# Optimization experiments

Hardware: AMD Instinct MI355X
Metric: run time of the kernel (lower is better)

The kernel has to match this reference:

```python
import jax, jax.numpy as jnp
import numpy as np

# ---------------- Chu-Liu-Edmonds MST decode (faithful numpy port) ----------------

def _find_cycle(parents, length, current_nodes):
    added = [False] * length
    added[0] = True
    cycle = set()
    has_cycle = False
    for i in range(1, length):
        if has_cycle:
            break
        if added[i] or not current_nodes[i]:
            continue
        this_cycle = {i}
        added[i] = True
        has_cycle = True
        next_node = i
        while parents[next_node] not in this_cycle:
            next_node = parents[next_node]
            if added[next_node]:
                has_cycle = False
                break
            added[next_node] = True
            this_cycle.add(next_node)
        if has_cycle:
            original = next_node
            cycle.add(original)
            next_node = parents[original]
            while next_node != original:
                cycle.add(next_node)
                next_node = parents[next_node]
            break
    return has_cycle, list(cycle)


def chu_liu_edmonds(length, score_matrix, current_nodes, final_edges, old_input, old_output, representatives):
    parents = [-1]
    for node1 in range(1, length):
        parents.append(0)
        if current_nodes[node1]:
            max_score = score_matrix[0, node1]
            for node2 in range(1, length):
                if node2 == node1 or not current_nodes[node2]:
                    continue
                new_score = score_matrix[node2, node1]
                if new_score > max_score:
                    max_score = new_score
                    parents[node1] = node2
    has_cycle, cycle = _find_cycle(parents, length, current_nodes)
    if not has_cycle:
        final_edges[0] = -1
        for node in range(1, length):
            if not current_nodes[node]:
                continue
            parent = old_input[parents[node], node]
            child = old_output[parents[node], node]
            final_edges[child] = parent
        return
    cycle_weight = 0.0
    for node in cycle:
        cycle_weight += score_matrix[parents[node], node]
    cycle_representative = cycle[0]
    for node in range(length):
        if not current_nodes[node] or node in cycle:
            continue
        in_edge_weight = float('-inf')
        in_edge = -1
        out_edge_weight = float('-inf')
        out_edge = -1
        for node_in_cycle in cycle:
            if score_matrix[node_in_cycle, node] > in_edge_weight:
                in_edge_weight = score_matrix[node_in_cycle, node]
                in_edge = node_in_cycle
            score = cycle_weight + score_matrix[node, node_in_cycle] - score_matrix[parents[node_in_cycle], node_in_cycle]
            if score > out_edge_weight:
                out_edge_weight = score
                out_edge = node_in_cycle
        score_matrix[cycle_representative, node] = in_edge_weight
        old_input[cycle_representative, node] = old_input[in_edge, node]
        old_output[cycle_representative, node] = old_output[in_edge, node]
        score_matrix[node, cycle_representative] = out_edge_weight
        old_output[node, cycle_representative] = old_output[node, out_edge]
        old_input[node, cycle_representative] = old_input[node, out_edge]
    considered = []
    for i, node_in_cycle in enumerate(cycle):
        considered.append(set())
        if i > 0:
            current_nodes[node_in_cycle] = False
        for node in representatives[node_in_cycle]:
            considered[i].add(node)
            if i > 0:
                representatives[cycle_representative].add(node)
    chu_liu_edmonds(length, score_matrix, current_nodes, final_edges, old_input, old_output, representatives)
    found = False
    key_node = -1
    for i, node in enumerate(cycle):
        for cycle_rep in considered[i]:
            if cycle_rep in final_edges:
                key_node = node
                found = True
                break
        if found:
            break
    previous = parents[key_node]
    while previous != key_node:
        child = old_output[parents[previous], previous]
        parent = old_input[parents[previous], previous]
        final_edges[child] = parent
        previous = parents[previous]


def decode_mst(energy, length):
    # energy: numpy [num_labels, T, T]
    max_length = energy.shape[-1]
    energy = energy[:, :length, :length]
    label_id_matrix = energy.argmax(axis=0)
    score_matrix = np.array(energy.max(axis=0), copy=True)
    old_input = np.zeros([length, length], dtype=np.int32)
    old_output = np.zeros([length, length], dtype=np.int32)
    current_nodes = [True] * length
    representatives = []
    for node1 in range(length):
        score_matrix[node1, node1] = 0.0
        representatives.append({node1})
        for node2 in range(node1 + 1, length):
            old_input[node1, node2] = node1
            old_output[node1, node2] = node2
            old_input[node2, node1] = node2
            old_output[node2, node1] = node1
    final_edges = {}
    chu_liu_edmonds(length, score_matrix, current_nodes, final_edges, old_input, old_output, representatives)
    heads = np.zeros([max_length], np.int32)
    head_type = np.ones([max_length], np.int32)
    for child, parent in final_edges.items():
        heads[child] = parent
        head_type[child] = label_id_matrix[parent, child]
    return heads, head_type


# ---------------- biaffine scoring (jax) ----------------

@jax.jit
def _energy(encoded_text, W_head_arc, b_head_arc, W_dep_arc, b_dep_arc, U_arc,
            W_head_lab, b_head_lab, W_dep_lab, b_dep_lab, U_lab):
    h_arc = jax.nn.elu(encoded_text @ W_head_arc + b_head_arc)   # [B,T,A]
    d_arc = jax.nn.elu(encoded_text @ W_dep_arc + b_dep_arc)     # [B,T,A]
    arc_scores = jnp.einsum('bia,ac,bjc->bij', h_arc, U_arc, d_arc)  # head i -> dep j
    h_lab = jax.nn.elu(encoded_text @ W_head_lab + b_head_lab)   # [B,T,R]
    d_lab = jax.nn.elu(encoded_text @ W_dep_lab + b_dep_lab)     # [B,T,R]
    lab_scores = jnp.einsum('bir,lrs,bjs->blij', h_lab, U_lab, d_lab)  # [B,L,T,T]
    norm_arc = jax.nn.log_softmax(arc_scores, axis=1)   # normalize over heads
    norm_lab = jax.nn.log_softmax(lab_scores, axis=1)   # normalize over labels
    return jnp.exp(norm_arc[:, None, :, :] + norm_lab)  # [B,L,T,T] edge energies


def setup_inputs() -> dict:
    key = jax.random.key(0)
    ks = jax.random.split(key, 8)
    B, T, D, A, R, L = 32, 128, 768, 512, 128, 50
    s = 0.02
    return {
        'encoded_text': jax.random.normal(ks[0], (B, T, D), jnp.float32),
        'W_head_arc': jax.random.normal(ks[1], (D, A), jnp.float32) * s,
        'b_head_arc': jnp.zeros((A,), jnp.float32),
        'W_dep_arc': jax.random.normal(ks[2], (D, A), jnp.float32) * s,
        'b_dep_arc': jnp.zeros((A,), jnp.float32),
        'U_arc': jax.random.normal(ks[3], (A, A), jnp.float32) * s,
        'W_head_lab': jax.random.normal(ks[4], (D, R), jnp.float32) * s,
        'b_head_lab': jnp.zeros((R,), jnp.float32),
        'W_dep_lab': jax.random.normal(ks[5], (D, R), jnp.float32) * s,
        'b_dep_lab': jnp.zeros((R,), jnp.float32),
        'U_lab': jax.random.normal(ks[6], (L, R, R), jnp.float32) * s,
        'mask': jnp.ones((B, T), jnp.bool_),
    }


def reference(encoded_text, W_head_arc, b_head_arc, W_dep_arc, b_dep_arc, U_arc,
              W_head_lab, b_head_lab, W_dep_lab, b_dep_lab, U_lab, mask):
    energy = _energy(encoded_text, W_head_arc, b_head_arc, W_dep_arc, b_dep_arc, U_arc,
                     W_head_lab, b_head_lab, W_dep_lab, b_dep_lab, U_lab)
    lengths = np.asarray(mask.sum(-1))
    energy_np = np.asarray(energy)
    heads, tags = [], []
    # per-example Chu-Liu-Edmonds decode (inherently sequential, as in the original)
    for i in range(energy_np.shape[0]):
        h, t = decode_mst(energy_np[i], int(lengths[i]))
        heads.append(h)
        tags.append(t)
    return energy, jnp.asarray(np.stack(heads)), jnp.asarray(np.stack(tags))
```

## Files before the change

### kernel.cpp

```cpp
#include <hip/hip_runtime.h>
#include <math.h>

#define B_ 32
#define T_ 128
#define D_ 768
#define A_ 512
#define R_ 128
#define L_ 50

__global__ __launch_bounds__(256)
void proj_gemm_k(const float* __restrict__ X,
                 const float* __restrict__ Wha, const float* __restrict__ bha,
                 const float* __restrict__ Wda, const float* __restrict__ bda,
                 const float* __restrict__ Whl, const float* __restrict__ bhl,
                 const float* __restrict__ Wdl, const float* __restrict__ bdl,
                 float* __restrict__ HA, float* __restrict__ DA,
                 float* __restrict__ HL, float* __restrict__ DL)
{
    __shared__ float As[16][68];
    __shared__ float Bs[16][132];
    const int bx = blockIdx.x;
    const float *W, *bias; float* C; int ld, ncol;
    if (bx < 4)      { W = Wha; bias = bha; C = HA; ld = 512; ncol = bx * 128; }
    else if (bx < 8) { W = Wda; bias = bda; C = DA; ld = 512; ncol = (bx - 4) * 128; }
    else if (bx == 8){ W = Whl; bias = bhl; C = HL; ld = 128; ncol = 0; }
    else             { W = Wdl; bias = bdl; C = DL; ld = 128; ncol = 0; }
    const int m0 = blockIdx.y * 64;
    const int tid = threadIdx.x;
    const int tx = tid & 15, ry = tid >> 4;
    float acc[4][8] = {};
    for (int k0 = 0; k0 < 768; k0 += 16) {
        {
            int row = tid >> 2, kb = (tid & 3) * 4;
            float4 a = *(const float4*)&X[(size_t)(m0 + row) * 768 + k0 + kb];
            As[kb + 0][row] = a.x; As[kb + 1][row] = a.y;
            As[kb + 2][row] = a.z; As[kb + 3][row] = a.w;
        }
        {
            int kk = tid >> 4, c0 = (tid & 15) * 4;
            const float* Bp = &W[(size_t)(k0 + kk) * ld + ncol + c0];
            *(float4*)&Bs[kk][c0] = *(const float4*)&Bp[0];
            *(float4*)&Bs[kk][c0 + 64] = *(const float4*)&Bp[64];
        }
        __syncthreads();
#pragma unroll
        for (int kk = 0; kk < 16; ++kk) {
            float4 a4 = *(const float4*)&As[kk][ry * 4];
            float4 b0 = *(const float4*)&Bs[kk][tx * 4];
            float4 b1 = *(const float4*)&Bs[kk][tx * 4 + 64];
            float av[4] = { a4.x, a4.y, a4.z, a4.w };
            float bv[8] = { b0.x, b0.y, b0.z, b0.w, b1.x, b1.y, b1.z, b1.w };
#pragma unroll
            for (int i = 0; i < 4; ++i)
#pragma unroll
                for (int j = 0; j < 8; ++j)
                    acc[i][j] += av[i] * bv[j];
        }
        __syncthreads();
    }
    float bv0[8];
    {
        float4 q0 = *(const float4*)&bias[ncol + tx * 4];
        float4 q1 = *(const float4*)&bias[ncol + tx * 4 + 64];
        bv0[0] = q0.x; bv0[1] = q0.y; bv0[2] = q0.z; bv0[3] = q0.w;
        bv0[4] = q1.x; bv0[5] = q1.y; bv0[6] = q1.z; bv0[7] = q1.w;
    }
#pragma unroll
    for (int i = 0; i < 4; ++i) {
        int m = m0 + ry * 4 + i;
        size_t base = (size_t)m * ld + ncol;
        float o[8];
#pragma unroll
        for (int j = 0; j < 8; ++j) {
            float v = acc[i][j] + bv0[j];
            o[j] = v > 0.0f ? v : expm1f(v);
        }
        float4 s0 = { o[0], o[1], o[2], o[3] };
        float4 s1 = { o[4], o[5], o[6], o[7] };
        *(float4*)&C[base + tx * 4] = s0;
        *(float4*)&C[base + tx * 4 + 64] = s1;
    }
}

__global__ __launch_bounds__(256)
void gemm_k(const float* __restrict__ A, const float* __restrict__ B,
            const float* __restrict__ bias, float* __restrict__ C,
            int K, int lda, int ldb, int ldc,
            long long sA, long long sB, long long sC, long long c_outer, int flags)
{
    __shared__ float As[16][68];
    __shared__ float Bs[16][132];
    A += (size_t)blockIdx.z * sA;
    B += (size_t)blockIdx.z * sB;
    C += (size_t)blockIdx.z * sC;
    const int m0 = blockIdx.y * 64, n0 = blockIdx.x * 128;
    const int tid = threadIdx.x;
    const int tx = tid & 15, ry = tid >> 4;
    float acc[4][8] = {};
    for (int k0 = 0; k0 < K; k0 += 16) {
        {
            int row = tid >> 2, kb = (tid & 3) * 4;
            float4 a = *(const float4*)&A[(size_t)(m0 + row) * lda + k0 + kb];
            As[kb + 0][row] = a.x; As[kb + 1][row] = a.y;
            As[kb + 2][row] = a.z; As[kb + 3][row] = a.w;
        }
        if (!(flags & 4)) {
            int kk = tid >> 4, c0 = (tid & 15) * 4;
            const float* Bp = &B[(size_t)(k0 + kk) * ldb + n0 + c0];
            *(float4*)&Bs[kk][c0] = *(const float4*)&Bp[0];
            *(float4*)&Bs[kk][c0 + 64] = *(const float4*)&Bp[64];
        } else {
            int col = tid >> 1, kb = (tid & 1) * 8;
            const float* Bp = &B[(size_t)(n0 + col) * ldb + k0 + kb];
            float4 b0 = *(const float4*)&Bp[0];
            float4 b1 = *(const float4*)&Bp[4];
            Bs[kb + 0][col] = b0.x; Bs[kb + 1][col] = b0.y;
            Bs[kb + 2][col] = b0.z; Bs[kb + 3][col] = b0.w;
            Bs[kb + 4][col] = b1.x; Bs[kb + 5][col] = b1.y;
            Bs[kb + 6][col] = b1.z; Bs[kb + 7][col] = b1.w;
        }
        __syncthreads();
#pragma unroll
        for (int kk = 0; kk < 16; ++kk) {
            float4 a4 = *(const float4*)&As[kk][ry * 4];
            float4 b0 = *(const float4*)&Bs[kk][tx * 4];
            float4 b1 = *(const float4*)&Bs[kk][tx * 4 + 64];
            float av[4] = { a4.x, a4.y, a4.z, a4.w };
            float bv[8] = { b0.x, b0.y, b0.z, b0.w, b1.x, b1.y, b1.z, b1.w };
#pragma unroll
            for (int i = 0; i < 4; ++i)
#pragma unroll
                for (int j = 0; j < 8; ++j)
                    acc[i][j] += av[i] * bv[j];
        }
        __syncthreads();
    }
    float bv0[8] = {};
    if (flags & 1) {
        float4 q0 = *(const float4*)&bias[n0 + tx * 4];
        float4 q1 = *(const float4*)&bias[n0 + tx * 4 + 64];
        bv0[0] = q0.x; bv0[1] = q0.y; bv0[2] = q0.z; bv0[3] = q0.w;
        bv0[4] = q1.x; bv0[5] = q1.y; bv0[6] = q1.z; bv0[7] = q1.w;
    }
#pragma unroll
    for (int i = 0; i < 4; ++i) {
        int m = m0 + ry * 4 + i;
        size_t base = (size_t)(m >> 7) * c_outer + (size_t)(m & 127) * ldc + n0;
        float o[8];
#pragma unroll
        for (int j = 0; j < 8; ++j) {
            float v = acc[i][j] + bv0[j];
            if (flags & 2) v = v > 0.0f ? v : expm1f(v);
            o[j] = v;
        }
        float4 s0 = { o[0], o[1], o[2], o[3] };
        float4 s1 = { o[4], o[5], o[6], o[7] };
        *(float4*)&C[base + tx * 4] = s0;
        *(float4*)&C[base + tx * 4 + 64] = s1;
    }
}

__global__ __launch_bounds__(256)
void transpose_k(const float* __restrict__ in, float* __restrict__ out)
{
    __shared__ float tile[32][33];
    int b = blockIdx.z;
    int bx = blockIdx.x, by = blockIdx.y;
    int tx = threadIdx.x, ty = threadIdx.y;
    const float* src = in + (size_t)b * T_ * R_;
    float* dst = out + (size_t)b * T_ * R_;
#pragma unroll
    for (int r = 0; r < 4; ++r)
        tile[ty + 8 * r][tx] = src[(size_t)(by * 32 + ty + 8 * r) * 128 + bx * 32 + tx];
    __syncthreads();
#pragma unroll
    for (int r = 0; r < 4; ++r)
        dst[(size_t)(bx * 32 + ty + 8 * r) * 128 + by * 32 + tx] = tile[tx][ty + 8 * r];
}

__global__ __launch_bounds__(128)
void arc_logsoftmax_k(float* __restrict__ arc)
{
    int b = blockIdx.x, j = threadIdx.x;
    float* base = arc + (size_t)b * T_ * T_ + j;
    float m = -INFINITY;
    for (int i = 0; i < T_; ++i) m = fmaxf(m, base[(size_t)i * T_]);
    float s = 0.0f;
    for (int i = 0; i < T_; ++i) s += expf(base[(size_t)i * T_] - m);
    float ls = m + logf(s);
    for (int i = 0; i < T_; ++i) base[(size_t)i * T_] -= ls;
}

__global__ __launch_bounds__(256)
void tl_lab_k(const float* __restrict__ HL, const float* __restrict__ Ul,
              const float* __restrict__ dlt, float* __restrict__ E)
{
    __shared__ float Ts[128 * 68];
    __shared__ float As[16][68];
    __shared__ float Bs[16][132];
    const int l = blockIdx.x, b = blockIdx.y;
    const int m0 = blockIdx.z * 64;
    const int tid = threadIdx.x;
    const int tx = tid & 15, ry = tid >> 4;
    const float* Apan = HL + (size_t)b * 16384 + (size_t)m0 * 128;
    const float* Bpan = Ul + (size_t)l * 16384;
    const float* Dpan = dlt + (size_t)b * 16384;
    float acc[4][8] = {};
    for (int k0 = 0; k0 < 128; k0 += 16) {
        {
            int row = tid >> 2, kb = (tid & 3) * 4;
            float4 a = *(const float4*)&Apan[(size_t)row * 128 + k0 + kb];
            As[kb + 0][row] = a.x; As[kb + 1][row] = a.y;
            As[kb + 2][row] = a.z; As[kb + 3][row] = a.w;
        }
        {
            int kk = tid >> 4, c0 = (tid & 15) * 4;
            const float* Bp = &Bpan[(size_t)(k0 + kk) * 128 + c0];
            *(float4*)&Bs[kk][c0] = *(const float4*)&Bp[0];
            *(float4*)&Bs[kk][c0 + 64] = *(const float4*)&Bp[64];
        }
        __syncthreads();
#pragma unroll
        for (int kk = 0; kk < 16; ++kk) {
            float4 a4 = *(const float4*)&As[kk][ry * 4];
            float4 b0 = *(const float4*)&Bs[kk][tx * 4];
            float4 b1 = *(const float4*)&Bs[kk][tx * 4 + 64];
            float av[4] = { a4.x, a4.y, a4.z, a4.w };
            float bv[8] = { b0.x, b0.y, b0.z, b0.w, b1.x, b1.y, b1.z, b1.w };
#pragma unroll
            for (int i = 0; i < 4; ++i)
#pragma unroll
                for (int j = 0; j < 8; ++j)
                    acc[i][j] += av[i] * bv[j];
        }
        __syncthreads();
    }
#pragma unroll
    for (int j = 0; j < 8; ++j) {
        int col = (j < 4) ? (tx * 4 + j) : (64 + tx * 4 + j - 4);
        float4 w = { acc[0][j], acc[1][j], acc[2][j], acc[3][j] };
        *(float4*)&Ts[col * 68 + ry * 4] = w;
#pragma unroll
        for (int i = 0; i < 4; ++i) acc[i][j] = 0.0f;
    }
    __syncthreads();
    for (int k0 = 0; k0 < 128; k0 += 16) {
        {
            int kk = tid >> 4, c0 = (tid & 15) * 4;
            const float* Bp = &Dpan[(size_t)(k0 + kk) * 128 + c0];
            *(float4*)&Bs[kk][c0] = *(const float4*)&Bp[0];
            *(float4*)&Bs[kk][c0 + 64] = *(const float4*)&Bp[64];
        }
        __syncthreads();
#pragma unroll
        for (int kk = 0; kk < 16; ++kk) {
            float4 a4 = *(const float4*)&Ts[(k0 + kk) * 68 + ry * 4];
            float4 b0 = *(const float4*)&Bs[kk][tx * 4];
            float4 b1 = *(const float4*)&Bs[kk][tx * 4 + 64];
            float av[4] = { a4.x, a4.y, a4.z, a4.w };
            float bv[8] = { b0.x, b0.y, b0.z, b0.w, b1.x, b1.y, b1.z, b1.w };
#pragma unroll
            for (int i = 0; i < 4; ++i)
#pragma unroll
                for (int j = 0; j < 8; ++j)
                    acc[i][j] += av[i] * bv[j];
        }
        __syncthreads();
    }
    float* base = E + ((size_t)b * L_ + l) * 16384 + (size_t)m0 * 128;
#pragma unroll
    for (int i = 0; i < 4; ++i) {
        float4 s0 = { acc[i][0], acc[i][1], acc[i][2], acc[i][3] };
        float4 s1 = { acc[i][4], acc[i][5], acc[i][6], acc[i][7] };
        *(float4*)&base[(size_t)(ry * 4 + i) * 128 + tx * 4] = s0;
        *(float4*)&base[(size_t)(ry * 4 + i) * 128 + tx * 4 + 64] = s1;
    }
}

__global__ __launch_bounds__(256)
void energy_combine_k(float* __restrict__ E, const float* __restrict__ narc,
                      float* __restrict__ score_g, unsigned char* __restrict__ labmax_g)
{
    int g = blockIdx.x * 256 + threadIdx.x;
    int b = g >> 14;
    int ij = g & 16383;
    float* base = E + (size_t)b * L_ * T_ * T_ + ij;
    float v[L_];
    float m = -INFINITY;
    int am = 0;
#pragma unroll
    for (int l = 0; l < L_; ++l) {
        v[l] = base[(size_t)l * T_ * T_];
        if (v[l] > m) { m = v[l]; am = l; }
    }
    float s = 0.0f;
#pragma unroll
    for (int l = 0; l < L_; ++l) s += expf(v[l] - m);
    float ls = m + logf(s);
    float na = narc[(size_t)b * T_ * T_ + ij];
#pragma unroll
    for (int l = 0; l < L_; ++l) base[(size_t)l * T_ * T_] = expf(na + v[l] - ls);
    int i = ij >> 7, j = ij & 127;
    score_g[(size_t)b * 16384 + ij] = (i == j) ? 0.0f : expf(na + m - ls);
    labmax_g[(size_t)b * 16384 + ij] = (unsigned char)am;
}

__global__ __launch_bounds__(256)
void mst_k(const float* __restrict__ score_g, const unsigned char* __restrict__ labmax_g,
           float* __restrict__ heads, float* __restrict__ tags)
{
    const int b = blockIdx.x, t = threadIdx.x;
    __shared__ float score[128 * 129];
    __shared__ unsigned short oio[128 * 129];
    __shared__ unsigned char pstL[96 * 128];
    __shared__ unsigned char kynL[96 * 128];
    __shared__ int parents[128];
    __shared__ int fe[128];
    __shared__ float pmx[128];
    __shared__ int pp[128];
    __shared__ float cwacc[128];
    __shared__ int cnt[128];
    __shared__ int offarr[128];
    __shared__ float Lsub[128];
    __shared__ unsigned char Lnode[128], Lcid[128];
    __shared__ unsigned char cidarr[128], oncyc[128];

    {
        const float4* src = (const float4*)(score_g + (size_t)b * 16384);
        for (int i = t; i < 4096; i += 256) {
            float4 v = src[i];
            int r = i >> 5, c = (i & 31) * 4;
            float* d = &score[r * 129 + c];
            d[0] = v.x; d[1] = v.y; d[2] = v.z; d[3] = v.w;
        }
    }
    for (int i = t; i < 16384; i += 256) {
        int r = i >> 7, c = i & 127;
        oio[r * 129 + c] = (unsigned short)(r | (c << 8));
    }
    if (t < 128) { fe[t] = -2; oncyc[t] = 0; }
    __syncthreads();
    if (t < 128) score[t * 129 + t] = -INFINITY;
    __syncthreads();
    float mxl = 0.0f; int pl = 0;
    if (t >= 128) {
        int col = t - 128;
        float mx = -INFINITY; int pu = 64;
        if (col != 0) {
            mx = score[64 * 129 + col];
#pragma unroll 16
            for (int n2 = 65; n2 < 128; ++n2) {
                float sc = score[n2 * 129 + col];
                if (sc > mx) { mx = sc; pu = n2; }
            }
        }
        pmx[col] = mx; pp[col] = pu;
    } else if (t != 0) {
        mxl = score[t]; pl = 0;
#pragma unroll 16
        for (int n2 = 1; n2 < 64; ++n2) {
            float sc = score[n2 * 129 + t];
            if (sc > mxl) { mxl = sc; pl = n2; }
        }
    }
    __syncthreads();
    if (t == 0) parents[0] = -1;
    else if (t < 128) parents[t] = (pmx[t] > mxl) ? pp[t] : pl;
    __syncthreads();

    if (t < 64) {
        const int n0 = t, n1 = t + 64;
        int p0 = parents[n0], p1 = parents[n1];
        int c0 = 1, c1 = 1;
        int r0 = n0, r1 = n1;
        int lev = 0, nact = 128, pass = 0;
        for (;;) {
            int rounds = 32 - __clz(nact - 1);
            int a0 = (n0 == 0 || !c0) ? 0 : p0;
            int a1 = (!c1) ? 0 : p1;
            int m0 = n0, m1 = n1;
            for (int s = 0; s < rounds; ++s) {
                int pk0 = (a0 << 7) | m0;
                int pk1 = (a1 << 7) | m1;
                int q00 = __shfl(pk0, a0 & 63, 64);
                int q01 = __shfl(pk1, a0 & 63, 64);
                int q10 = __shfl(pk0, a1 & 63, 64);
                int q11 = __shfl(pk1, a1 & 63, 64);
                int g0 = (a0 & 64) ? q01 : q00;
                int g1 = (a1 & 64) ? q11 : q10;
                a0 = g0 >> 7; int gm0 = g0 & 127; m0 = gm0 < m0 ? gm0 : m0;
                a1 = g1 >> 7; int gm1 = g1 & 127; m1 = gm1 < m1 ? gm1 : m1;
            }
            int pred0 = (n0 >= 1) && c0 && (a0 != 0);
            int pred1 = c1 && (a1 != 0);
            unsigned long long bal0 = __ballot(pred0);
            unsigned long long bal1 = __ballot(pred1);
            if (bal0 == 0ull && bal1 == 0ull) {
                if (n0 == 0) fe[0] = -1;
                else if (c0) { int w = oio[p0 * 129 + n0]; fe[w >> 8] = w & 255; }
                if (c1) { int w = oio[p1 * 129 + n1]; fe[w >> 8] = w & 255; }
                __threadfence_block();
                break;
            }
            unsigned char ep = (unsigned char)(++pass);
            if (pred0) oncyc[a0] = ep;
            if (pred1) oncyc[a1] = ep;
            cnt[n0] = 0; cnt[n1] = 0;
            cwacc[n0] = 0.0f; cwacc[n1] = 0.0f;
            __threadfence_block();
            int onc0 = c0 && (oncyc[n0] == ep);
            int onc1 = c1 && (oncyc[n1] == ep);
            const int cid0 = m0, cid1 = m1;
            cidarr[n0] = onc0 ? (unsigned char)cid0 : 0xFF;
            cidarr[n1] = onc1 ? (unsigned char)cid1 : 0xFF;
            float sub0 = 0.0f, sub1 = 0.0f;
            int rk0 = 0, rk1 = 0;
            if (onc0) { sub0 = score[p0 * 129 + n0]; rk0 = atomicAdd(&cnt[cid0], 1); atomicAdd(&cwacc[cid0], sub0); }
            if (onc1) { sub1 = score[p1 * 129 + n1]; rk1 = atomicAdd(&cnt[cid1], 1); atomicAdd(&cwacc[cid1], sub1); }
            __threadfence_block();
            int x0 = cnt[n0], x1 = cnt[n1];
            int v = (x0 & 0xFFFF) | (x1 << 16);
            for (int off = 1; off < 64; off <<= 1) {
                int u = __shfl(v, t >= off ? t - off : 0, 64);
                v += (t >= off) ? u : 0;
            }
            int tot = __shfl(v, 63, 64);
            int Mtot = (tot & 0xFFFF) + (tot >> 16);
            offarr[n0] = (v & 0xFFFF) - x0;
            offarr[n1] = (tot & 0xFFFF) + ((v >> 16) & 0xFFFF) - x1;
            __threadfence_block();
            if (onc0) { int sl = offarr[cid0] + rk0; Lnode[sl] = (unsigned char)n0; Lcid[sl] = (unsigned char)cid0; Lsub[sl] = sub0; }
            if (onc1) { int sl = offarr[cid1] + rk1; Lnode[sl] = (unsigned char)n1; Lcid[sl] = (unsigned char)cid1; Lsub[sl] = sub1; }
            int rc0 = cidarr[r0], rc1 = cidarr[r1];
            if (lev < 96) {
                pstL[lev * 128 + n0] = (unsigned char)p0;
                pstL[lev * 128 + n1] = (unsigned char)p1;
                kynL[lev * 128 + n0] = (rc0 != 0xFF) ? (unsigned char)r0 : 0xFF;
                kynL[lev * 128 + n1] = (rc1 != 0xFF) ? (unsigned char)r1 : 0xFF;
            }
            if (rc0 != 0xFF) r0 = rc0;
            if (rc1 != 0xFF) r1 = rc1;
            __threadfence_block();
            {
                int lim0 = c0 ? (onc0 ? cid0 : 256) : -1;
                int lim1 = c1 ? (onc1 ? cid1 : 256) : -1;
                float inw0 = -INFINITY, outw0 = -INFINITY;
                float inw1 = -INFINITY, outw1 = -INFINITY;
                int qi0 = 0, qo0 = 0, qi1 = 0, qo1 = 0;
                int cidC = Lcid[0], mC = Lnode[0];
                float sbC = Lsub[0];
                for (int i = 0; i < Mtot; ++i) {
                    int cidN = 0, mN = 0; float sbN = 0.0f;
                    if (i + 1 < Mtot) { cidN = Lcid[i + 1]; mN = Lnode[i + 1]; sbN = Lsub[i + 1]; }
                    if (cidC < lim0) {
                        float si = score[mC * 129 + n0];
                        float so = score[n0 * 129 + mC] - sbC;
                        int wi = oio[mC * 129 + n0];
                        int wo = oio[n0 * 129 + mC];
                        if (si > inw0) { inw0 = si; qi0 = wi; }
                        if (so > outw0) { outw0 = so; qo0 = wo; }
                    }
                    if (cidC < lim1) {
                        float si = score[mC * 129 + n1];
                        float so = score[n1 * 129 + mC] - sbC;
                        int wi = oio[mC * 129 + n1];
                        int wo = oio[n1 * 129 + mC];
                        if (si > inw1) { inw1 = si; qi1 = wi; }
                        if (so > outw1) { outw1 = so; qo1 = wo; }
                    }
                    int segend = (i + 1 == Mtot) || (cidN != cidC);
                    if (segend) {
                        if (cidC < lim0) {
                            float cwc = cwacc[cidC];
                            score[cidC * 129 + n0] = inw0; oio[cidC * 129 + n0] = (unsigned short)qi0;
                            score[n0 * 129 + cidC] = cwc + outw0; oio[n0 * 129 + cidC] = (unsigned short)qo0;
                        }
                        if (cidC < lim1) {
                            float cwc = cwacc[cidC];
                            score[cidC * 129 + n1] = inw1; oio[cidC * 129 + n1] = (unsigned short)qi1;
                            score[n1 * 129 + cidC] = cwc + outw1; oio[n1 * 129 + cidC] = (unsigned short)qo1;
                        }
                        inw0 = -INFINITY; outw0 = -INFINITY;
                        inw1 = -INFINITY; outw1 = -INFINITY;
                    }
                    cidC = cidN; mC = mN; sbC = sbN;
                }
            }
            __threadfence_block();
            int rp0 = onc0 && (n0 == cid0);
            int rp1 = onc1 && (n1 == cid1);
            unsigned long long q0 = __ballot(rp0);
            unsigned long long q1 = __ballot(rp1);
            int ncyc = (int)__popcll(q0) + (int)__popcll(q1);
            if (ncyc >= 2) {
                float inw0 = -INFINITY, outw0 = -INFINITY;
                float inw1 = -INFINITY, outw1 = -INFINITY;
                int qi0 = 0, qo0 = 0, qi1 = 0, qo1 = 0;
                int cidC = Lcid[0], mC = Lnode[0];
                float sbC = Lsub[0];
                for (int i = 0; i < Mtot; ++i) {
                    int cidN = 0, mN = 0; float sbN = 0.0f;
                    if (i + 1 < Mtot) { cidN = Lcid[i + 1]; mN = Lnode[i + 1]; sbN = Lsub[i + 1]; }
                    int e0 = rp0 && (cidC > cid0);
                    int e1 = rp1 && (cidC > cid1);
                    if (e0) {
                        float si = score[mC * 129 + n0];
                        float so = score[n0 * 129 + mC] - sbC;
                        int wi = oio[mC * 129 + n0];
                        int wo = oio[n0 * 129 + mC];
                        if (si > inw0) { inw0 = si; qi0 = wi; }
                        if (so > outw0) { outw0 = so; qo0 = wo; }
                    }
                    if (e1) {
                        float si = score[mC * 129 + n1];
                        float so = score[n1 * 129 + mC] - sbC;
                        int wi = oio[mC * 129 + n1];
                        int wo = oio[n1 * 129 + mC];
                        if (si > inw1) { inw1 = si; qi1 = wi; }
                        if (so > outw1) { outw1 = so; qo1 = wo; }
                    }
                    int segend = (i + 1 == Mtot) || (cidN != cidC);
                    if (segend) {
                        if (e0) {
                            float cwc = cwacc[cidC];
                            score[cidC * 129 + n0] = inw0; oio[cidC * 129 + n0] = (unsigned short)qi0;
                            score[n0 * 129 + cidC] = cwc + outw0; oio[n0 * 129 + cidC] = (unsigned short)qo0;
                        }
                        if (e1) {
                            float cwc = cwacc[cidC];
                            score[cidC * 129 + n1] = inw1; oio[cidC * 129 + n1] = (unsigned short)qi1;
                            score[n1 * 129 + cidC] = cwc + outw1; oio[n1 * 129 + cidC] = (unsigned short)qo1;
                        }
                        inw0 = -INFINITY; outw0 = -INFINITY;
                        inw1 = -INFINITY; outw1 = -INFINITY;
                    }
                    cidC = cidN; mC = mN; sbC = sbN;
                }
                __threadfence_block();
            }
            if (onc0 && n0 != cid0) c0 = 0;
            if (onc1 && n1 != cid1) c1 = 0;
            if (c0 && n0 != 0) { int cp = cidarr[p0]; if (cp != 0xFF) p0 = cp; }
            if (c1)            { int cp = cidarr[p1]; if (cp != 0xFF) p1 = cp; }
            {
                unsigned long long w0 = q0, w1 = q1;
                while (w0 | w1) {
                    int repA, repB = -1;
                    if (w0) { repA = (int)__ffsll((long long)w0) - 1; w0 &= w0 - 1; }
                    else    { repA = 64 + (int)__ffsll((long long)w1) - 1; w1 &= w1 - 1; }
                    if (w0) { repB = (int)__ffsll((long long)w0) - 1; w0 &= w0 - 1; }
                    else if (w1) { repB = 64 + (int)__ffsll((long long)w1) - 1; w1 &= w1 - 1; }
                    float aA = c0 ? score[n0 * 129 + repA] : -INFINITY;
                    float bA = c1 ? score[n1 * 129 + repA] : -INFINITY;
                    float aB = -INFINITY, bB = -INFINITY;
                    if (repB >= 0) {
                        aB = c0 ? score[n0 * 129 + repB] : -INFINITY;
                        bB = c1 ? score[n1 * 129 + repB] : -INFINITY;
                    }
                    float vA; int iA;
                    if (bA > aA) { vA = bA; iA = n1; } else { vA = aA; iA = n0; }
                    float vB; int iB;
                    if (bB > aB) { vB = bB; iB = n1; } else { vB = aB; iB = n0; }
#pragma unroll
                    for (int off = 32; off >= 1; off >>= 1) {
                        float oA = __shfl_xor(vA, off, 64);
                        int jA = __shfl_xor(iA, off, 64);
                        float oB = __shfl_xor(vB, off, 64);
                        int jB = __shfl_xor(iB, off, 64);
                        if (oA > vA || (oA == vA && jA < iA)) { vA = oA; iA = jA; }
                        if (oB > vB || (oB == vB && jB < iB)) { vB = oB; iB = jB; }
                    }
                    if (n0 == repA) p0 = iA;
                    if (n1 == repA) p1 = iA;
                    if (repB >= 0) {
                        if (n0 == repB) p0 = iB;
                        if (n1 == repB) p1 = iB;
                    }
                }
            }
            nact -= (Mtot - ncyc);
            ++lev;
        }
        int ltop = lev < 96 ? lev : 96;
        for (int l2 = ltop - 1; l2 >= 0; --l2) {
            int ky0 = kynL[l2 * 128 + n0], ky1 = kynL[l2 * 128 + n1];
            int cand0 = (ky0 != 0xFF) && (fe[n0] != -2);
            int cand1 = (ky1 != 0xFF) && (fe[n1] != -2);
            if (cand0) {
                int key = ky0;
                int prev = pstL[l2 * 128 + key];
                int guard = 0;
                while (prev != key && guard++ < 130) {
                    int pp2 = pstL[l2 * 128 + prev];
                    int w = oio[pp2 * 129 + prev];
                    fe[w >> 8] = w & 255;
                    prev = pp2;
                }
            }
            if (cand1) {
                int key = ky1;
                int prev = pstL[l2 * 128 + key];
                int guard = 0;
                while (prev != key && guard++ < 130) {
                    int pp2 = pstL[l2 * 128 + prev];
                    int w = oio[pp2 * 129 + prev];
                    fe[w >> 8] = w & 255;
                    prev = pp2;
                }
            }
            __threadfence_block();
        }
    }
    __syncthreads();

    if (t < 128) {
        int f = fe[t];
        float h, ht;
        if (f != -2) {
            h = (float)f;
            int prow = (f < 0) ? 127 : f;
            ht = (float)(int)labmax_g[(size_t)b * 16384 + prow * 128 + t];
        } else { h = 0.0f; ht = 1.0f; }
        heads[b * 128 + t] = h;
        tags[b * 128 + t] = ht;
    }
}

extern "C" void kernel_launch(void* const* d_in, const int* in_sizes, int n_in,
                              void* d_out, int out_size, void* d_ws, size_t ws_size,
                              hipStream_t stream)
{
    const float* X   = (const float*)d_in[0];
    const float* Wha = (const float*)d_in[1];
    const float* bha = (const float*)d_in[2];
    const float* Wda = (const float*)d_in[3];
    const float* bda = (const float*)d_in[4];
    const float* Ua  = (const float*)d_in[5];
    const float* Whl = (const float*)d_in[6];
    const float* bhl = (const float*)d_in[7];
    const float* Wdl = (const float*)d_in[8];
    const float* bdl = (const float*)d_in[9];
    const float* Ul  = (const float*)d_in[10];

    char* ws = (char*)d_ws;
    float* HA    = (float*)(ws + (size_t)0);
    float* DA    = (float*)(ws + ((size_t)8 << 20));
    float* TA    = (float*)(ws + ((size_t)16 << 20));
    float* HL    = (float*)(ws + ((size_t)24 << 20));
    float* DL    = (float*)(ws + ((size_t)26 << 20));
    float* DLt   = (float*)(ws + ((size_t)28 << 20));
    float* ARC   = (float*)(ws + ((size_t)30 << 20));
    float* SCORE = (float*)(ws + ((size_t)32 << 20));
    unsigned char* LABMAX = (unsigned char*)(ws + ((size_t)34 << 20));

    float* E     = (float*)d_out;
    float* heads = E + (size_t)B_ * L_ * T_ * T_;
    float* tags  = heads + (size_t)B_ * T_;

    dim3 thr(256);
    proj_gemm_k<<<dim3(10, 64), thr, 0, stream>>>(X, Wha, bha, Wda, bda, Whl, bhl, Wdl, bdl,
                                                  HA, DA, HL, DL);
    gemm_k<<<dim3(4, 64, 1), thr, 0, stream>>>(HA, Ua, nullptr, TA, 512, 512, 512, 512, 0, 0, 0, (long long)128 * 512, 0);
    transpose_k<<<dim3(4, 4, 32), dim3(32, 8), 0, stream>>>(DL, DLt);
    gemm_k<<<dim3(1, 2, 32), thr, 0, stream>>>(TA, DA, nullptr, ARC, 512, 512, 512, 128, 65536, 65536, 16384, 0, 4);
    arc_logsoftmax_k<<<32, 128, 0, stream>>>(ARC);
    tl_lab_k<<<dim3(50, 32, 2), thr, 0, stream>>>(HL, Ul, DLt, E);
    energy_combine_k<<<2048, 256, 0, stream>>>(E, ARC, SCORE, LABMAX);
    mst_k<<<32, 256, 0, stream>>>(SCORE, LABMAX, heads, tags);
}
```

Measured before the change: 882.6 us.

## Unroll contraction scan by four and compute new cycle-rep parents per lane

Packs the per-member node and cycle-id lists into one 16-bit array padded with sentinel entries. The contraction scans are unrolled by four with all shared-memory loads issued up front, to expose memory-level parallelism. Parent selection for new cycle representatives changes from a wave-wide shuffle reduction per pair of reps to one lane per representative doing a serial 128-entry column scan. A compacted representative list is built with ballots. This trades shuffle reductions for per-lane serial loops and adds register pressure and redundant loads past segment ends.

After: 1.242 ms. 1.41x slower.

```diff
diff --git a/kernel.cpp b/kernel.cpp
--- a/kernel.cpp
+++ b/kernel.cpp
@@ -321,9 +321,9 @@
     __shared__ float cwacc[128];
     __shared__ int cnt[128];
     __shared__ int offarr[128];
-    __shared__ float Lsub[128];
-    __shared__ unsigned char Lnode[128], Lcid[128];
-    __shared__ unsigned char cidarr[128], oncyc[128];
+    __shared__ float Lsub[136];
+    __shared__ unsigned short Lpk[136];
+    __shared__ unsigned char cidarr[128], oncyc[128], replist[72];
 
     {
         const float4* src = (const float4*)(score_g + (size_t)b * 16384);
@@ -374,6 +374,7 @@
         int c0 = 1, c1 = 1;
         int r0 = n0, r1 = n1;
         int lev = 0, nact = 128, pass = 0;
+        const unsigned long long lmask = (1ull << t) - 1ull;
         for (;;) {
             int rounds = 32 - __clz(nact - 1);
             int a0 = (n0 == 0 || !c0) ? 0 : p0;
@@ -413,6 +414,13 @@
             const int cid0 = m0, cid1 = m1;
             cidarr[n0] = onc0 ? (unsigned char)cid0 : 0xFF;
             cidarr[n1] = onc1 ? (unsigned char)cid1 : 0xFF;
+            int rp0 = onc0 && (n0 == cid0);
+            int rp1 = onc1 && (n1 == cid1);
+            unsigned long long q0 = __ballot(rp0);
+            unsigned long long q1 = __ballot(rp1);
+            int ncyc = (int)__popcll(q0) + (int)__popcll(q1);
+            if (rp0) replist[(int)__popcll(q0 & lmask)] = (unsigned char)n0;
+            if (rp1) replist[(int)__popcll(q0) + (int)__popcll(q1 & lmask)] = (unsigned char)n1;
             float sub0 = 0.0f, sub1 = 0.0f;
             int rk0 = 0, rk1 = 0;
             if (onc0) { sub0 = score[p0 * 129 + n0]; rk0 = atomicAdd(&cnt[cid0], 1); atomicAdd(&cwacc[cid0], sub0); }
@@ -429,8 +437,9 @@
             offarr[n0] = (v & 0xFFFF) - x0;
             offarr[n1] = (tot & 0xFFFF) + ((v >> 16) & 0xFFFF) - x1;
             __threadfence_block();
-            if (onc0) { int sl = offarr[cid0] + rk0; Lnode[sl] = (unsigned char)n0; Lcid[sl] = (unsigned char)cid0; Lsub[sl] = sub0; }
-            if (onc1) { int sl = offarr[cid1] + rk1; Lnode[sl] = (unsigned char)n1; Lcid[sl] = (unsigned char)cid1; Lsub[sl] = sub1; }
+            if (onc0) { int sl = offarr[cid0] + rk0; Lpk[sl] = (unsigned short)(n0 | (cid0 << 8)); Lsub[sl] = sub0; }
+            if (onc1) { int sl = offarr[cid1] + rk1; Lpk[sl] = (unsigned short)(n1 | (cid1 << 8)); Lsub[sl] = sub1; }
+            if (t < 4) { Lpk[Mtot + t] = (unsigned short)(255 << 8); Lsub[Mtot + t] = 0.0f; }
             int rc0 = cidarr[r0], rc1 = cidarr[r1];
             if (lev < 96) {
                 pstL[lev * 128 + n0] = (unsigned char)p0;
@@ -442,99 +451,243 @@
             if (rc1 != 0xFF) r1 = rc1;
             __threadfence_block();
             {
-                int lim0 = c0 ? (onc0 ? cid0 : 256) : -1;
-                int lim1 = c1 ? (onc1 ? cid1 : 256) : -1;
+                int lim0 = c0 ? (onc0 ? cid0 : 128) : -1;
+                int lim1 = c1 ? (onc1 ? cid1 : 128) : -1;
                 float inw0 = -INFINITY, outw0 = -INFINITY;
                 float inw1 = -INFINITY, outw1 = -INFINITY;
                 int qi0 = 0, qo0 = 0, qi1 = 0, qo1 = 0;
-                int cidC = Lcid[0], mC = Lnode[0];
-                float sbC = Lsub[0];
-                for (int i = 0; i < Mtot; ++i) {
-                    int cidN = 0, mN = 0; float sbN = 0.0f;
-                    if (i + 1 < Mtot) { cidN = Lcid[i + 1]; mN = Lnode[i + 1]; sbN = Lsub[i + 1]; }
-                    if (cidC < lim0) {
-                        float si = score[mC * 129 + n0];
-                        float so = score[n0 * 129 + mC] - sbC;
-                        int wi = oio[mC * 129 + n0];
-                        int wo = oio[n0 * 129 + mC];
-                        if (si > inw0) { inw0 = si; qi0 = wi; }
-                        if (so > outw0) { outw0 = so; qo0 = wo; }
-                    }
-                    if (cidC < lim1) {
-                        float si = score[mC * 129 + n1];
-                        float so = score[n1 * 129 + mC] - sbC;
-                        int wi = oio[mC * 129 + n1];
-                        int wo = oio[n1 * 129 + mC];
-                        if (si > inw1) { inw1 = si; qi1 = wi; }
-                        if (so > outw1) { outw1 = so; qo1 = wo; }
-                    }
-                    int segend = (i + 1 == Mtot) || (cidN != cidC);
-                    if (segend) {
-                        if (cidC < lim0) {
-                            float cwc = cwacc[cidC];
-                            score[cidC * 129 + n0] = inw0; oio[cidC * 129 + n0] = (unsigned short)qi0;
-                            score[n0 * 129 + cidC] = cwc + outw0; oio[n0 * 129 + cidC] = (unsigned short)qo0;
-                        }
-                        if (cidC < lim1) {
-                            float cwc = cwacc[cidC];
-                            score[cidC * 129 + n1] = inw1; oio[cidC * 129 + n1] = (unsigned short)qi1;
-                            score[n1 * 129 + cidC] = cwc + outw1; oio[n1 * 129 + cidC] = (unsigned short)qo1;
-                        }
-                        inw0 = -INFINITY; outw0 = -INFINITY;
-                        inw1 = -INFINITY; outw1 = -INFINITY;
-                    }
-                    cidC = cidN; mC = mN; sbC = sbN;
+                for (int i = 0; i < Mtot; i += 4) {
+                    int pkA = Lpk[i], pkB = Lpk[i + 1], pkC = Lpk[i + 2], pkD = Lpk[i + 3];
+                    int dE = Lpk[i + 4] >> 8;
+                    float sbA = Lsub[i], sbB = Lsub[i + 1], sbC = Lsub[i + 2], sbD = Lsub[i + 3];
+                    int uA = pkA & 255, dA = pkA >> 8;
+                    int uB = pkB & 255, dB = pkB >> 8;
+                    int uC = pkC & 255, dC = pkC >> 8;
+                    int uD = pkD & 255, dD = pkD >> 8;
+                    float siA0 = score[uA * 129 + n0], soA0 = score[n0 * 129 + uA];
+                    float siA1 = score[uA * 129 + n1], soA1 = score[n1 * 129 + uA];
+                    int wiA0 = oio[uA * 129 + n0], woA0 = oio[n0 * 129 + uA];
+                    int wiA1 = oio[uA * 129 + n1], woA1 = oio[n1 * 129 + uA];
+                    float siB0 = score[uB * 129 + n0], soB0 = score[n0 * 129 + uB];
+                    float siB1 = score[uB * 129 + n1], soB1 = score[n1 * 129 + uB];
+                    int wiB0 = oio[uB * 129 + n0], woB0 = oio[n0 * 129 + uB];
+                    int wiB1 = oio[uB * 129 + n1], woB1 = oio[n1 * 129 + uB];
+                    float siC0 = score[uC * 129 + n0], soC0 = score[n0 * 129 + uC];
+                    float siC1 = score[uC * 129 + n1], soC1 = score[n1 * 129 + uC];
+                    int wiC0 = oio[uC * 129 + n0], woC0 = oio[n0 * 129 + uC];
+                    int wiC1 = oio[uC * 129 + n1], woC1 = oio[n1 * 129 + uC];
+                    float siD0 = score[uD * 129 + n0], soD0 = score[n0 * 129 + uD];
+                    float siD1 = score[uD * 129 + n1], soD1 = score[n1 * 129 + uD];
+                    int wiD0 = oio[uD * 129 + n0], woD0 = oio[n0 * 129 + uD];
+                    int wiD1 = oio[uD * 129 + n1], woD1 = oio[n1 * 129 + uD];
+                    float cwA = cwacc[dA & 127], cwB = cwacc[dB & 127];
+                    float cwC = cwacc[dC & 127], cwD = cwacc[dD & 127];
+                    if (dA < lim0) {
+                        if (siA0 > inw0) { inw0 = siA0; qi0 = wiA0; }
+                        float so = soA0 - sbA;
+                        if (so > outw0) { outw0 = so; qo0 = woA0; }
+                    }
+                    if (dA < lim1) {
+                        if (siA1 > inw1) { inw1 = siA1; qi1 = wiA1; }
+                        float so = soA1 - sbA;
+                        if (so > outw1) { outw1 = so; qo1 = woA1; }
+                    }
+                    if (dB != dA) {
+                        if (dA < lim0) {
+                            score[dA * 129 + n0] = inw0; oio[dA * 129 + n0] = (unsigned short)qi0;
+                            score[n0 * 129 + dA] = cwA + outw0; oio[n0 * 129 + dA] = (unsigned short)qo0;
+                        }
+                        if (dA < lim1) {
+                            score[dA * 129 + n1] = inw1; oio[dA * 129 + n1] = (unsigned short)qi1;
+                            score[n1 * 129 + dA] = cwA + outw1; oio[n1 * 129 + dA] = (unsigned short)qo1;
+                        }
+                        inw0 = -INFINITY; outw0 = -INFINITY; inw1 = -INFINITY; outw1 = -INFINITY;
+                    }
+                    if (dB < lim0) {
+                        if (siB0 > inw0) { inw0 = siB0; qi0 = wiB0; }
+                        float so = soB0 - sbB;
+                        if (so > outw0) { outw0 = so; qo0 = woB0; }
+                    }
+                    if (dB < lim1) {
+                        if (siB1 > inw1) { inw1 = siB1; qi1 = wiB1; }
+                        float so = soB1 - sbB;
+                        if (so > outw1) { outw1 = so; qo1 = woB1; }
+                    }
+                    if (dC != dB) {
+                        if (dB < lim0) {
+                            score[dB * 129 + n0] = inw0; oio[dB * 129 + n0] = (unsigned short)qi0;
+                            score[n0 * 129 + dB] = cwB + outw0; oio[n0 * 129 + dB] = (unsigned short)qo0;
+                        }
+                        if (dB < lim1) {
+                            score[dB * 129 + n1] = inw1; oio[dB * 129 + n1] = (unsigned short)qi1;
+                            score[n1 * 129 + dB] = cwB + outw1; oio[n1 * 129 + dB] = (unsigned short)qo1;
+                        }
+                        inw0 = -INFINITY; outw0 = -INFINITY; inw1 = -INFINITY; outw1 = -INFINITY;
+                    }
+                    if (dC < lim0) {
+                        if (siC0 > inw0) { inw0 = siC0; qi0 = wiC0; }
+                        float so = soC0 - sbC;
+                        if (so > outw0) { outw0 = so; qo0 = woC0; }
+                    }
+                    if (dC < lim1) {
+                        if (siC1 > inw1) { inw1 = siC1; qi1 = wiC1; }
+                        float so = soC1 - sbC;
+                        if (so > outw1) { outw1 = so; qo1 = woC1; }
+                    }
+                    if (dD != dC) {
+                        if (dC < lim0) {
+                            score[dC * 129 + n0] = inw0; oio[dC * 129 + n0] = (unsigned short)qi0;
+                            score[n0 * 129 + dC] = cwC + outw0; oio[n0 * 129 + dC] = (unsigned short)qo0;
+                        }
+                        if (dC < lim1) {
+                            score[dC * 129 + n1] = inw1; oio[dC * 129 + n1] = (unsigned short)qi1;
+                            score[n1 * 129 + dC] = cwC + outw1; oio[n1 * 129 + dC] = (unsigned short)qo1;
+                        }
+                        inw0 = -INFINITY; outw0 = -INFINITY; inw1 = -INFINITY; outw1 = -INFINITY;
+                    }
+                    if (dD < lim0) {
+                        if (siD0 > inw0) { inw0 = siD0; qi0 = wiD0; }
+                        float so = soD0 - sbD;
+                        if (so > outw0) { outw0 = so; qo0 = woD0; }
+                    }
+                    if (dD < lim1) {
+                        if (siD1 > inw1) { inw1 = siD1; qi1 = wiD1; }
+                        float so = soD1 - sbD;
+                        if (so > outw1) { outw1 = so; qo1 = woD1; }
+                    }
+                    if (dE != dD) {
+                        if (dD < lim0) {
+                            score[dD * 129 + n0] = inw0; oio[dD * 129 + n0] = (unsigned short)qi0;
+                            score[n0 * 129 + dD] = cwD + outw0; oio[n0 * 129 + dD] = (unsigned short)qo0;
+                        }
+                        if (dD < lim1) {
+                            score[dD * 129 + n1] = inw1; oio[dD * 129 + n1] = (unsigned short)qi1;
+                            score[n1 * 129 + dD] = cwD + outw1; oio[n1 * 129 + dD] = (unsigned short)qo1;
+                        }
+                        inw0 = -INFINITY; outw0 = -INFINITY; inw1 = -INFINITY; outw1 = -INFINITY;
+                    }
                 }
             }
             __threadfence_block();
-            int rp0 = onc0 && (n0 == cid0);
-            int rp1 = onc1 && (n1 == cid1);
-            unsigned long long q0 = __ballot(rp0);
-            unsigned long long q1 = __ballot(rp1);
-            int ncyc = (int)__popcll(q0) + (int)__popcll(q1);
             if (ncyc >= 2) {
                 float inw0 = -INFINITY, outw0 = -INFINITY;
                 float inw1 = -INFINITY, outw1 = -INFINITY;
                 int qi0 = 0, qo0 = 0, qi1 = 0, qo1 = 0;
-                int cidC = Lcid[0], mC = Lnode[0];
-                float sbC = Lsub[0];
-                for (int i = 0; i < Mtot; ++i) {
-                    int cidN = 0, mN = 0; float sbN = 0.0f;
-                    if (i + 1 < Mtot) { cidN = Lcid[i + 1]; mN = Lnode[i + 1]; sbN = Lsub[i + 1]; }
-                    int e0 = rp0 && (cidC > cid0);
-                    int e1 = rp1 && (cidC > cid1);
-                    if (e0) {
-                        float si = score[mC * 129 + n0];
-                        float so = score[n0 * 129 + mC] - sbC;
-                        int wi = oio[mC * 129 + n0];
-                        int wo = oio[n0 * 129 + mC];
-                        if (si > inw0) { inw0 = si; qi0 = wi; }
-                        if (so > outw0) { outw0 = so; qo0 = wo; }
-                    }
-                    if (e1) {
-                        float si = score[mC * 129 + n1];
-                        float so = score[n1 * 129 + mC] - sbC;
-                        int wi = oio[mC * 129 + n1];
-                        int wo = oio[n1 * 129 + mC];
-                        if (si > inw1) { inw1 = si; qi1 = wi; }
-                        if (so > outw1) { outw1 = so; qo1 = wo; }
-                    }
-                    int segend = (i + 1 == Mtot) || (cidN != cidC);
-                    if (segend) {
-                        if (e0) {
-                            float cwc = cwacc[cidC];
-                            score[cidC * 129 + n0] = inw0; oio[cidC * 129 + n0] = (unsigned short)qi0;
-                            score[n0 * 129 + cidC] = cwc + outw0; oio[n0 * 129 + cidC] = (unsigned short)qo0;
-                        }
-                        if (e1) {
-                            float cwc = cwacc[cidC];
-                            score[cidC * 129 + n1] = inw1; oio[cidC * 129 + n1] = (unsigned short)qi1;
-                            score[n1 * 129 + cidC] = cwc + outw1; oio[n1 * 129 + cidC] = (unsigned short)qo1;
-                        }
-                        inw0 = -INFINITY; outw0 = -INFINITY;
-                        inw1 = -INFINITY; outw1 = -INFINITY;
-                    }
-                    cidC = cidN; mC = mN; sbC = sbN;
+                int lo0 = rp0 ? cid0 : 999, lo1 = rp1 ? cid1 : 999;
+                for (int i = 0; i < Mtot; i += 4) {
+                    int pkA = Lpk[i], pkB = Lpk[i + 1], pkC = Lpk[i + 2], pkD = Lpk[i + 3];
+                    int dE = Lpk[i + 4] >> 8;
+                    float sbA = Lsub[i], sbB = Lsub[i + 1], sbC = Lsub[i + 2], sbD = Lsub[i + 3];
+                    int uA = pkA & 255, dA = pkA >> 8;
+                    int uB = pkB & 255, dB = pkB >> 8;
+                    int uC = pkC & 255, dC = pkC >> 8;
+                    int uD = pkD & 255, dD = pkD >> 8;
+                    float siA0 = score[uA * 129 + n0], soA0 = score[n0 * 129 + uA];
+                    float siA1 = score[uA * 129 + n1], soA1 = score[n1 * 129 + uA];
+                    int wiA0 = oio[uA * 129 + n0], woA0 = oio[n0 * 129 + uA];
+                    int wiA1 = oio[uA * 129 + n1], woA1 = oio[n1 * 129 + uA];
+                    float siB0 = score[uB * 129 + n0], soB0 = score[n0 * 129 + uB];
+                    float siB1 = score[uB * 129 + n1], soB1 = score[n1 * 129 + uB];
+                    int wiB0 = oio[uB * 129 + n0], woB0 = oio[n0 * 129 + uB];
+                    int wiB1 = oio[uB * 129 + n1], woB1 = oio[n1 * 129 + uB];
+                    float siC0 = score[uC * 129 + n0], soC0 = score[n0 * 129 + uC];
+                    float siC1 = score[uC * 129 + n1], soC1 = score[n1 * 129 + uC];
+                    int wiC0 = oio[uC * 129 + n0], woC0 = oio[n0 * 129 + uC];
+                    int wiC1 = oio[uC * 129 + n1], woC1 = oio[n1 * 129 + uC];
+                    float siD0 = score[uD * 129 + n0], soD0 = score[n0 * 129 + uD];
+                    float siD1 = score[uD * 129 + n1], soD1 = score[n1 * 129 + uD];
+                    int wiD0 = oio[uD * 129 + n0], woD0 = oio[n0 * 129 + uD];
+                    int wiD1 = oio[uD * 129 + n1], woD1 = oio[n1 * 129 + uD];
+                    float cwA = cwacc[dA & 127], cwB = cwacc[dB & 127];
+                    float cwC = cwacc[dC & 127], cwD = cwacc[dD & 127];
+                    int eA0 = (dA < 255) && (dA > lo0), eA1 = (dA < 255) && (dA > lo1);
+                    if (eA0) {
+                        if (siA0 > inw0) { inw0 = siA0; qi0 = wiA0; }
+                        float so = soA0 - sbA;
+                        if (so > outw0) { outw0 = so; qo0 = woA0; }
+                    }
+                    if (eA1) {
+                        if (siA1 > inw1) { inw1 = siA1; qi1 = wiA1; }
+                        float so = soA1 - sbA;
+                        if (so > outw1) { outw1 = so; qo1 = woA1; }
+                    }
+                    if (dB != dA) {
+                        if (eA0) {
+                            score[dA * 129 + n0] = inw0; oio[dA * 129 + n0] = (unsigned short)qi0;
+                            score[n0 * 129 + dA] = cwA + outw0; oio[n0 * 129 + dA] = (unsigned short)qo0;
+                        }
+                        if (eA1) {
+                            score[dA * 129 + n1] = inw1; oio[dA * 129 + n1] = (unsigned short)qi1;
+                            score[n1 * 129 + dA] = cwA + outw1; oio[n1 * 129 + dA] = (unsigned short)qo1;
+                        }
+                        inw0 = -INFINITY; outw0 = -INFINITY; inw1 = -INFINITY; outw1 = -INFINITY;
+                    }
+                    int eB0 = (dB < 255) && (dB > lo0), eB1 = (dB < 255) && (dB > lo1);
+                    if (eB0) {
+                        if (siB0 > inw0) { inw0 = siB0; qi0 = wiB0; }
+                        float so = soB0 - sbB;
+                        if (so > outw0) { outw0 = so; qo0 = woB0; }
+                    }
+                    if (eB1) {
+                        if (siB1 > inw1) { inw1 = siB1; qi1 = wiB1; }
+                        float so = soB1 - sbB;
+                        if (so > outw1) { outw1 = so; qo1 = woB1; }
+                    }
+                    if (dC != dB) {
+                        if (eB0) {
+                            score[dB * 129 + n0] = inw0; oio[dB * 129 + n0] = (unsigned short)qi0;
+                            score[n0 * 129 + dB] = cwB + outw0; oio[n0 * 129 + dB] = (unsigned short)qo0;
+                        }
+                        if (eB1) {
+                            score[dB * 129 + n1] = inw1; oio[dB * 129 + n1] = (unsigned short)qi1;
+                            score[n1 * 129 + dB] = cwB + outw1; oio[n1 * 129 + dB] = (unsigned short)qo1;
+                        }
+                        inw0 = -INFINITY; outw0 = -INFINITY; inw1 = -INFINITY; outw1 = -INFINITY;
+                    }
+                    int eC0 = (dC < 255) && (dC > lo0), eC1 = (dC < 255) && (dC > lo1);
+                    if (eC0) {
+                        if (siC0 > inw0) { inw0 = siC0; qi0 = wiC0; }
+                        float so = soC0 - sbC;
+                        if (so > outw0) { outw0 = so; qo0 = woC0; }
+                    }
+                    if (eC1) {
+                        if (siC1 > inw1) { inw1 = siC1; qi1 = wiC1; }
+                        float so = soC1 - sbC;
+                        if (so > outw1) { outw1 = so; qo1 = woC1; }
+                    }
+                    if (dD != dC) {
+                        if (eC0) {
+                            score[dC * 129 + n0] = inw0; oio[dC * 129 + n0] = (unsigned short)qi0;
+                            score[n0 * 129 + dC] = cwC + outw0; oio[n0 * 129 + dC] = (unsigned short)qo0;
+                        }
+                        if (eC1) {
+                            score[dC * 129 + n1] = inw1; oio[dC * 129 + n1] = (unsigned short)qi1;
+                            score[n1 * 129 + dC] = cwC + outw1; oio[n1 * 129 + dC] = (unsigned short)qo1;
+                        }
+                        inw0 = -INFINITY; outw0 = -INFINITY; inw1 = -INFINITY; outw1 = -INFINITY;
+                    }
+                    int eD0 = (dD < 255) && (dD > lo0), eD1 = (dD < 255) && (dD > lo1);
+                    if (eD0) {
+                        if (siD0 > inw0) { inw0 = siD0; qi0 = wiD0; }
+                        float so = soD0 - sbD;
+                        if (so > outw0) { outw0 = so; qo0 = woD0; }
+                    }
+                    if (eD1) {
+                        if (siD1 > inw1) { inw1 = siD1; qi1 = wiD1; }
+                        float so = soD1 - sbD;
+                        if (so > outw1) { outw1 = so; qo1 = woD1; }
+                    }
+                    if (dE != dD) {
+                        if (eD0) {
+                            score[dD * 129 + n0] = inw0; oio[dD * 129 + n0] = (unsigned short)qi0;
+                            score[n0 * 129 + dD] = cwD + outw0; oio[n0 * 129 + dD] = (unsigned short)qo0;
+                        }
+                        if (eD1) {
+                            score[dD * 129 + n1] = inw1; oio[dD * 129 + n1] = (unsigned short)qi1;
+                            score[n1 * 129 + dD] = cwD + outw1; oio[n1 * 129 + dD] = (unsigned short)qo1;
+                        }
+                        inw0 = -INFINITY; outw0 = -INFINITY; inw1 = -INFINITY; outw1 = -INFINITY;
+                    }
                 }
                 __threadfence_block();
             }
@@ -543,40 +696,24 @@
             if (c0 && n0 != 0) { int cp = cidarr[p0]; if (cp != 0xFF) p0 = cp; }
             if (c1)            { int cp = cidarr[p1]; if (cp != 0xFF) p1 = cp; }
             {
-                unsigned long long w0 = q0, w1 = q1;
-                while (w0 | w1) {
-                    int repA, repB = -1;
-                    if (w0) { repA = (int)__ffsll((long long)w0) - 1; w0 &= w0 - 1; }
-                    else    { repA = 64 + (int)__ffsll((long long)w1) - 1; w1 &= w1 - 1; }
-                    if (w0) { repB = (int)__ffsll((long long)w0) - 1; w0 &= w0 - 1; }
-                    else if (w1) { repB = 64 + (int)__ffsll((long long)w1) - 1; w1 &= w1 - 1; }
-                    float aA = c0 ? score[n0 * 129 + repA] : -INFINITY;
-                    float bA = c1 ? score[n1 * 129 + repA] : -INFINITY;
-                    float aB = -INFINITY, bB = -INFINITY;
-                    if (repB >= 0) {
-                        aB = c0 ? score[n0 * 129 + repB] : -INFINITY;
-                        bB = c1 ? score[n1 * 129 + repB] : -INFINITY;
-                    }
-                    float vA; int iA;
-                    if (bA > aA) { vA = bA; iA = n1; } else { vA = aA; iA = n0; }
-                    float vB; int iB;
-                    if (bB > aB) { vB = bB; iB = n1; } else { vB = aB; iB = n0; }
-#pragma unroll
-                    for (int off = 32; off >= 1; off >>= 1) {
-                        float oA = __shfl_xor(vA, off, 64);
-                        int jA = __shfl_xor(iA, off, 64);
-                        float oB = __shfl_xor(vB, off, 64);
-                        int jB = __shfl_xor(iB, off, 64);
-                        if (oA > vA || (oA == vA && jA < iA)) { vA = oA; iA = jA; }
-                        if (oB > vB || (oB == vB && jB < iB)) { vB = oB; iB = jB; }
-                    }
-                    if (n0 == repA) p0 = iA;
-                    if (n1 == repA) p1 = iA;
-                    if (repB >= 0) {
-                        if (n0 == repB) p0 = iB;
-                        if (n1 == repB) p1 = iB;
-                    }
+                unsigned long long am0 = __ballot(c0);
+                unsigned long long am1 = __ballot(c1);
+                if (t < ncyc) {
+                    int rep = replist[t];
+                    float mx = score[rep];
+                    int par = 0;
+#pragma unroll 4
+                    for (int x = 1; x < 128; ++x) {
+                        int alive = (x < 64) ? (int)((am0 >> x) & 1ull)
+                                             : (int)((am1 >> (x - 64)) & 1ull);
+                        float sc = score[x * 129 + rep];
+                        if (alive && x != rep && sc > mx) { mx = sc; par = x; }
+                    }
+                    pp[rep] = par;
                 }
+                __threadfence_block();
+                if (c0 && onc0) p0 = pp[n0];
+                if (c1 && onc1) p1 = pp[n1];
             }
             nact -= (Mtot - ncyc);
             ++lev;
```
